# Kernel optimization log

Measured on AMD Instinct MI355X. Metric: run time of the kernel, lower is better.

Reference implementation:

```python
import jax, jax.numpy as jnp
import numpy as np

B, I, H = 65536, 128, 256


def setup_inputs() -> dict:
    key = jax.random.key(0)
    ks = jax.random.split(key, 8)
    return {
        "x_t": jax.random.normal(ks[0], (B, I), dtype=jnp.float32),
        "delta_t": jax.random.uniform(ks[1], (B, 1), dtype=jnp.float32),
        "h_prev": jax.random.normal(ks[2], (B, H), dtype=jnp.float32),
        "c_prev": jax.random.normal(ks[3], (B, H), dtype=jnp.float32),
        # stacked gate weights, order: s, f, i, T, u, o
        "Wh": jax.random.normal(ks[4], (6, H, H), dtype=jnp.float32) * 0.05,
        "Wx": jax.random.normal(ks[5], (6, H, I), dtype=jnp.float32) * 0.05,
        # s_t-input weights, order: f, i, T, u, o
        "Ws": jax.random.normal(ks[6], (5, H, H), dtype=jnp.float32) * 0.05,
        "Wst": jax.random.normal(ks[7], (H, 1), dtype=jnp.float32) * 0.05,
        "b": jnp.zeros((6, H), dtype=jnp.float32),
    }


def reference(x_t, delta_t, h_prev, c_prev, Wh, Wx, Ws, Wst, b):
    # Batched GEMMs over the 6 gates (nn.Linear: y = x @ W.T)
    pre_h = jnp.einsum('bi,goi->gbo', h_prev, Wh)      # [6,B,H]
    pre_x = jnp.einsum('bi,goi->gbo', x_t, Wx)         # [6,B,H]
    s_t = jnp.tanh(pre_h[0] + pre_x[0] + delta_t @ Wst.T + b[0])
    pre_s = jnp.einsum('bi,goi->gbo', s_t, Ws)         # [5,B,H]
    g = pre_h[1:] + pre_x[1:] + pre_s + b[1:, None, :]  # [5,B,H] f,i,T,u,o
    f_t = jax.nn.sigmoid(g[0])
    i_t = jax.nn.sigmoid(g[1])
    T_t = jax.nn.sigmoid(g[2])
    zeta = jnp.tanh(g[3])
    o_t = jax.nn.sigmoid(g[4])
    c_t = f_t * c_prev + i_t * zeta + T_t * s_t
    h_tilde = o_t * jnp.tanh(c_t)
    return (h_tilde, c_t)
```

## Files before the change

### kernel.cpp

```cpp
#include <hip/hip_runtime.h>
#include <hip/hip_bf16.h>


constexpr int Btot = 65536;
constexpr int H    = 256;
constexpr int I    = 128;
constexpr int K1   = 384;
constexpr int BT   = 32;
constexpr int NTHR = 512;
constexpr int SOFF = 24576;

typedef __bf16 bf16x8  __attribute__((ext_vector_type(8)));
typedef float  f32x16  __attribute__((ext_vector_type(16)));
typedef float  f32x4v  __attribute__((ext_vector_type(4)));
typedef unsigned short ushort8 __attribute__((ext_vector_type(8)));

__device__ __forceinline__ unsigned short f2bf(float f) {
    unsigned u = __builtin_bit_cast(unsigned, f);
    u += 0x7fffu + ((u >> 16) & 1u);
    return (unsigned short)(u >> 16);
}
__device__ __forceinline__ float bf2f(unsigned short s) {
    return __builtin_bit_cast(float, ((unsigned)s) << 16);
}
__device__ __forceinline__ float sigm(float x) {
    return __builtin_amdgcn_rcpf(1.0f + exp2f(-1.4426950408889634f * x));
}
__device__ __forceinline__ float tanh_f(float x) {
    return 1.0f - 2.0f * __builtin_amdgcn_rcpf(1.0f + exp2f(2.8853900817779268f * x));
}

__global__ void convert_w(const float* __restrict__ Wh, const float* __restrict__ Wx,
                          const float* __restrict__ Ws, unsigned short* __restrict__ w0,
                          unsigned short* __restrict__ wg) {
    const int t  = blockIdx.x * blockDim.x + threadIdx.x;
    const int N0 = 48 * 2048;
    const int N1 = 5 * 80 * 2048;
    if (t < N0) {
        const int k8 = t >> 11, rem = t & 2047;
        const int col = rem >> 3, e = rem & 7;
        const int k = k8 * 8 + e;
        const float v = (k < H) ? Wh[col * H + k] : Wx[col * I + (k - H)];
        w0[t] = f2bf(v);
    } else if (t < N0 + N1) {
        const int u   = t - N0;
        const int g1  = u / 163840;
        const int rem = u - g1 * 163840;
        const int k8  = rem >> 11;
        const int r2  = rem & 2047;
        const int col = r2 >> 3, e = r2 & 7;
        const int k   = k8 * 8 + e;
        const int g   = g1 + 1;
        float v;
        if (k < H)        v = Wh[g * H * H + col * H + k];
        else if (k < K1)  v = Wx[g * H * I + col * I + (k - H)];
        else              v = Ws[g1 * H * H + col * H + (k - K1)];
        wg[u] = f2bf(v);
    }
}

template<int NIT>
__device__ __forceinline__ void gemm1(const unsigned char* Ab, int abase,
        const unsigned short* __restrict__ Wp, f32x16& acc) {
    bf16x8 b[2], a[2];
    #pragma unroll
    for (int i = 0; i < 2; ++i) {
        b[i] = *(const bf16x8*)(Wp + i * 4096);
        a[i] = *(const bf16x8*)(Ab + abase + i * 1024);
    }
    #pragma unroll
    for (int i = 0; i < NIT; ++i) {
        const bf16x8 av = a[i & 1], bv = b[i & 1];
        if (i + 2 < NIT) {
            a[i & 1] = *(const bf16x8*)(Ab + abase + (i + 2) * 1024);
            b[i & 1] = *(const bf16x8*)(Wp + (i + 2) * 4096);
        }
        acc = __builtin_amdgcn_mfma_f32_32x32x16_bf16(av, bv, acc, 0, 0, 0);
    }
}

__global__ __launch_bounds__(NTHR, 4) void thlstm_fused(
        const float* __restrict__ x_t, const float* __restrict__ delta_t,
        const float* __restrict__ h_prev, const float* __restrict__ c_prev,
        const float* __restrict__ Wst, const float* __restrict__ bias,
        const unsigned short* __restrict__ w0, const unsigned short* __restrict__ wg,
        float* __restrict__ out) {
    __shared__ __align__(16) unsigned char Abuf[40960];
    const int tid = threadIdx.x;
    const int b0  = blockIdx.x * BT;

    #pragma unroll
    for (int it = 0; it < 3; ++it) {
        const int c   = it * NTHR + tid;
        const int k8  = c >> 5, row = c & 31;
        const float* src = (k8 < 32) ? (h_prev + (size_t)(b0 + row) * H + k8 * 8)
                                     : (x_t    + (size_t)(b0 + row) * I + (k8 - 32) * 8);
        const f32x4v v0 = __builtin_nontemporal_load((const f32x4v*)src);
        const f32x4v v1 = __builtin_nontemporal_load(((const f32x4v*)src) + 1);
        ushort8 p;
        p[0] = f2bf(v0[0]); p[1] = f2bf(v0[1]); p[2] = f2bf(v0[2]); p[3] = f2bf(v0[3]);
        p[4] = f2bf(v1[0]); p[5] = f2bf(v1[1]); p[6] = f2bf(v1[2]); p[7] = f2bf(v1[3]);
        *(ushort8*)(Abuf + (k8 * 32 + row) * 16) = p;
    }
    __syncthreads();

    const int lane  = tid & 63;
    const int wv    = tid >> 6;
    const int half  = lane >> 5;
    const int l31   = lane & 31;
    const int ocol  = wv * 32 + l31;
    const int rbase = 4 * half;
    const int abase = half * 512 + l31 * 16;
    const int wlo   = half * 2048 + ocol * 8;
    const int sbase = SOFF + ((ocol >> 3) * 32) * 16 + (ocol & 7) * 2;

    {
        f32x16 acc;
        #pragma unroll
        for (int r = 0; r < 16; ++r) acc[r] = 0.f;
        gemm1<24>(Abuf, abase, w0 + wlo, acc);
        const float wst = Wst[ocol];
        const float bs  = bias[ocol];
        #pragma unroll
        for (int r = 0; r < 16; ++r) {
            const int mrow = (r & 3) + 8 * (r >> 2) + rbase;
            const float sv = tanh_f(acc[r] + delta_t[b0 + mrow] * wst + bs);
            *(unsigned short*)(Abuf + sbase + mrow * 16) = f2bf(sv);
        }
    }
    __syncthreads();

    float    cacc[16];
    unsigned ipk[8];

    {
        f32x16 ac;
        #pragma unroll
        for (int r = 0; r < 16; ++r) ac[r] = 0.f;
        gemm1<40>(Abuf, abase, wg + 0 * 163840 + wlo, ac);
        const float bg = bias[1 * H + ocol];
        #pragma unroll
        for (int r = 0; r < 16; ++r) {
            const int mrow = (r & 3) + 8 * (r >> 2) + rbase;
            const size_t idx = (size_t)(b0 + mrow) * H + ocol;
            cacc[r] = sigm(ac[r] + bg) * __builtin_nontemporal_load(&c_prev[idx]);
        }
    }
    {
        f32x16 ac;
        #pragma unroll
        for (int r = 0; r < 16; ++r) ac[r] = 0.f;
        gemm1<40>(Abuf, abase, wg + 2 * 163840 + wlo, ac);
        const float bg = bias[3 * H + ocol];
        #pragma unroll
        for (int r = 0; r < 16; ++r) {
            const int mrow = (r & 3) + 8 * (r >> 2) + rbase;
            const float sv = bf2f(*(const unsigned short*)(Abuf + sbase + mrow * 16));
            cacc[r] += sigm(ac[r] + bg) * sv;
        }
    }
    {
        f32x16 ac;
        #pragma unroll
        for (int r = 0; r < 16; ++r) ac[r] = 0.f;
        gemm1<40>(Abuf, abase, wg + 1 * 163840 + wlo, ac);
        const float bg = bias[2 * H + ocol];
        float tmpf = 0.f;
        #pragma unroll
        for (int r = 0; r < 16; ++r) {
            const float sg = sigm(ac[r] + bg);
            if ((r & 1) == 0) tmpf = sg;
            else ipk[r >> 1] = (unsigned)f2bf(tmpf) | ((unsigned)f2bf(sg) << 16);
        }
    }
    {
        f32x16 ac;
        #pragma unroll
        for (int r = 0; r < 16; ++r) ac[r] = 0.f;
        gemm1<40>(Abuf, abase, wg + 3 * 163840 + wlo, ac);
        const float bg = bias[4 * H + ocol];
        #pragma unroll
        for (int r = 0; r < 16; ++r) {
            const float iv = bf2f((unsigned short)((ipk[r >> 1] >> ((r & 1) * 16)) & 0xffffu));
            cacc[r] += iv * tanh_f(ac[r] + bg);
        }
    }
    {
        f32x16 ac;
        #pragma unroll
        for (int r = 0; r < 16; ++r) ac[r] = 0.f;
        gemm1<40>(Abuf, abase, wg + 4 * 163840 + wlo, ac);
        const float bg = bias[5 * H + ocol];
        #pragma unroll
        for (int r = 0; r < 16; ++r) {
            const int mrow = (r & 3) + 8 * (r >> 2) + rbase;
            const size_t idx = (size_t)(b0 + mrow) * H + ocol;
            const float c = cacc[r];
            __builtin_nontemporal_store(sigm(ac[r] + bg) * tanh_f(c), &out[idx]);
            __builtin_nontemporal_store(c, &out[(size_t)Btot * H + idx]);
        }
    }
}

extern "C" void kernel_launch(void* const* d_in, const int* in_sizes, int n_in,
                              void* d_out, int out_size, void* d_ws, size_t ws_size,
                              hipStream_t stream) {
    (void)in_sizes; (void)n_in; (void)out_size; (void)ws_size;
    const float* x_t    = (const float*)d_in[0];
    const float* delta  = (const float*)d_in[1];
    const float* h_prev = (const float*)d_in[2];
    const float* c_prev = (const float*)d_in[3];
    const float* Wh     = (const float*)d_in[4];
    const float* Wx     = (const float*)d_in[5];
    const float* Ws     = (const float*)d_in[6];
    const float* Wst    = (const float*)d_in[7];
    const float* bias   = (const float*)d_in[8];
    float* out = (float*)d_out;

    unsigned short* w0 = (unsigned short*)d_ws;
    unsigned short* wg = w0 + 48 * 2048;

    const int total = 48 * 2048 + 5 * 80 * 2048;
    convert_w<<<(total + 255) / 256, 256, 0, stream>>>(Wh, Wx, Ws, w0, wg);
    thlstm_fused<<<Btot / BT, NTHR, 0, stream>>>(x_t, delta, h_prev, c_prev,
                                                 Wst, bias, w0, wg, out);
}
```

Before: 211.3 us.

## Split GEMM K dimension across wave pairs with LDS partial-sum exchange

Doubles the block to 1024 threads and splits each gate GEMM's K dimension between two waves that share the same output columns. Partial accumulators are written to LDS as bf16, exchanged after a barrier, and each wave finishes half the rows of the epilogue. The aim is shorter per-wave MFMA chains and more waves to hide latency. In exchange it adds a barrier per gate, LDS traffic, bf16 rounding of the partial sums, and raises LDS use to about 104KB, which limits occupancy to one block per CU.

New measurement: 353.9 us. 1.67x slower.

```diff
diff --git a/kernel.cpp b/kernel.cpp
--- a/kernel.cpp
+++ b/kernel.cpp
@@ -7,8 +7,9 @@
 constexpr int I    = 128;
 constexpr int K1   = 384;
 constexpr int BT   = 32;
-constexpr int NTHR = 512;
+constexpr int NTHR = 1024;
 constexpr int SOFF = 24576;
+constexpr int POFF = 40960;
 
 typedef __bf16 bf16x8  __attribute__((ext_vector_type(8)));
 typedef float  f32x16  __attribute__((ext_vector_type(16)));
@@ -79,124 +80,160 @@
     }
 }
 
+__device__ __forceinline__ void combine(unsigned char* Ab, const f32x16& acc,
+        int pw0, int pw1, int prd, int ks, int pp, float full[8]) {
+    ushort8 p0, p1;
+    #pragma unroll
+    for (int j = 0; j < 8; ++j) { p0[j] = f2bf(acc[j]); p1[j] = f2bf(acc[8 + j]); }
+    *(ushort8*)(Ab + pp * 32768 + pw0) = p0;
+    *(ushort8*)(Ab + pp * 32768 + pw1) = p1;
+    __syncthreads();
+    const ushort8 q = *(const ushort8*)(Ab + pp * 32768 + prd);
+    #pragma unroll
+    for (int j = 0; j < 8; ++j) full[j] = acc[ks * 8 + j] + bf2f(q[j]);
+}
+
 __global__ __launch_bounds__(NTHR, 4) void thlstm_fused(
         const float* __restrict__ x_t, const float* __restrict__ delta_t,
         const float* __restrict__ h_prev, const float* __restrict__ c_prev,
         const float* __restrict__ Wst, const float* __restrict__ bias,
         const unsigned short* __restrict__ w0, const unsigned short* __restrict__ wg,
         float* __restrict__ out) {
-    __shared__ __align__(16) unsigned char Abuf[40960];
+    __shared__ __align__(16) unsigned char Abuf[106496];
     const int tid = threadIdx.x;
     const int b0  = blockIdx.x * BT;
 
     #pragma unroll
-    for (int it = 0; it < 3; ++it) {
-        const int c   = it * NTHR + tid;
-        const int k8  = c >> 5, row = c & 31;
-        const float* src = (k8 < 32) ? (h_prev + (size_t)(b0 + row) * H + k8 * 8)
-                                     : (x_t    + (size_t)(b0 + row) * I + (k8 - 32) * 8);
-        const f32x4v v0 = __builtin_nontemporal_load((const f32x4v*)src);
-        const f32x4v v1 = __builtin_nontemporal_load(((const f32x4v*)src) + 1);
-        ushort8 p;
-        p[0] = f2bf(v0[0]); p[1] = f2bf(v0[1]); p[2] = f2bf(v0[2]); p[3] = f2bf(v0[3]);
-        p[4] = f2bf(v1[0]); p[5] = f2bf(v1[1]); p[6] = f2bf(v1[2]); p[7] = f2bf(v1[3]);
-        *(ushort8*)(Abuf + (k8 * 32 + row) * 16) = p;
+    for (int it = 0; it < 2; ++it) {
+        const int c = it * NTHR + tid;
+        if (c < BT * 48) {
+            const int k8 = c >> 5, row = c & 31;
+            const float* src = (k8 < 32) ? (h_prev + (size_t)(b0 + row) * H + k8 * 8)
+                                         : (x_t    + (size_t)(b0 + row) * I + (k8 - 32) * 8);
+            const f32x4v v0 = __builtin_nontemporal_load((const f32x4v*)src);
+            const f32x4v v1 = __builtin_nontemporal_load(((const f32x4v*)src) + 1);
+            ushort8 p;
+            p[0] = f2bf(v0[0]); p[1] = f2bf(v0[1]); p[2] = f2bf(v0[2]); p[3] = f2bf(v0[3]);
+            p[4] = f2bf(v1[0]); p[5] = f2bf(v1[1]); p[6] = f2bf(v1[2]); p[7] = f2bf(v1[3]);
+            *(ushort8*)(Abuf + (k8 * 32 + row) * 16) = p;
+        }
     }
     __syncthreads();
 
     const int lane  = tid & 63;
     const int wv    = tid >> 6;
+    const int cs    = wv >> 1;
+    const int ks    = wv & 1;
     const int half  = lane >> 5;
     const int l31   = lane & 31;
-    const int ocol  = wv * 32 + l31;
+    const int ocol  = cs * 32 + l31;
     const int rbase = 4 * half;
     const int abase = half * 512 + l31 * 16;
     const int wlo   = half * 2048 + ocol * 8;
-    const int sbase = SOFF + ((ocol >> 3) * 32) * 16 + (ocol & 7) * 2;
-
-    {
-        f32x16 acc;
-        #pragma unroll
-        for (int r = 0; r < 16; ++r) acc[r] = 0.f;
-        gemm1<24>(Abuf, abase, w0 + wlo, acc);
+    const int sbase = SOFF + (ocol >> 3) * 512 + (ocol & 7) * 2;
+    const int pw0 = POFF + wv * 1024 + lane * 16;
+    const int pw1 = POFF + 16384 + wv * 1024 + lane * 16;
+    const int prd = POFF + ks * 16384 + (wv ^ 1) * 1024 + lane * 16;
+
+    {
+        f32x16 acc;
+        #pragma unroll
+        for (int r = 0; r < 16; ++r) acc[r] = 0.f;
+        gemm1<12>(Abuf, abase + ks * 12 * 1024, w0 + wlo + ks * 12 * 4096, acc);
+        float full[8];
+        combine(Abuf, acc, pw0, pw1, prd, ks, 0, full);
         const float wst = Wst[ocol];
         const float bs  = bias[ocol];
         #pragma unroll
-        for (int r = 0; r < 16; ++r) {
-            const int mrow = (r & 3) + 8 * (r >> 2) + rbase;
-            const float sv = tanh_f(acc[r] + delta_t[b0 + mrow] * wst + bs);
+        for (int j = 0; j < 8; ++j) {
+            const int r = ks * 8 + j;
+            const int mrow = (r & 3) + 8 * (r >> 2) + rbase;
+            const float sv = tanh_f(full[j] + delta_t[b0 + mrow] * wst + bs);
             *(unsigned short*)(Abuf + sbase + mrow * 16) = f2bf(sv);
         }
     }
     __syncthreads();
 
-    float    cacc[16];
-    unsigned ipk[8];
-
-    {
-        f32x16 ac;
-        #pragma unroll
-        for (int r = 0; r < 16; ++r) ac[r] = 0.f;
-        gemm1<40>(Abuf, abase, wg + 0 * 163840 + wlo, ac);
+    float    cacc[8];
+    unsigned ipk[4];
+
+    {
+        f32x16 acc;
+        #pragma unroll
+        for (int r = 0; r < 16; ++r) acc[r] = 0.f;
+        gemm1<20>(Abuf, abase + ks * 20 * 1024, wg + 0 * 163840 + wlo + ks * 20 * 4096, acc);
+        float full[8];
+        combine(Abuf, acc, pw0, pw1, prd, ks, 1, full);
         const float bg = bias[1 * H + ocol];
         #pragma unroll
-        for (int r = 0; r < 16; ++r) {
+        for (int j = 0; j < 8; ++j) {
+            const int r = ks * 8 + j;
             const int mrow = (r & 3) + 8 * (r >> 2) + rbase;
             const size_t idx = (size_t)(b0 + mrow) * H + ocol;
-            cacc[r] = sigm(ac[r] + bg) * __builtin_nontemporal_load(&c_prev[idx]);
-        }
-    }
-    {
-        f32x16 ac;
-        #pragma unroll
-        for (int r = 0; r < 16; ++r) ac[r] = 0.f;
-        gemm1<40>(Abuf, abase, wg + 2 * 163840 + wlo, ac);
+            cacc[j] = sigm(full[j] + bg) * __builtin_nontemporal_load(&c_prev[idx]);
+        }
+    }
+    {
+        f32x16 acc;
+        #pragma unroll
+        for (int r = 0; r < 16; ++r) acc[r] = 0.f;
+        gemm1<20>(Abuf, abase + ks * 20 * 1024, wg + 2 * 163840 + wlo + ks * 20 * 4096, acc);
+        float full[8];
+        combine(Abuf, acc, pw0, pw1, prd, ks, 0, full);
         const float bg = bias[3 * H + ocol];
         #pragma unroll
-        for (int r = 0; r < 16; ++r) {
+        for (int j = 0; j < 8; ++j) {
+            const int r = ks * 8 + j;
             const int mrow = (r & 3) + 8 * (r >> 2) + rbase;
             const float sv = bf2f(*(const unsigned short*)(Abuf + sbase + mrow * 16));
-            cacc[r] += sigm(ac[r] + bg) * sv;
-        }
-    }
-    {
-        f32x16 ac;
-        #pragma unroll
-        for (int r = 0; r < 16; ++r) ac[r] = 0.f;
-        gemm1<40>(Abuf, abase, wg + 1 * 163840 + wlo, ac);
+            cacc[j] += sigm(full[j] + bg) * sv;
+        }
+    }
+    {
+        f32x16 acc;
+        #pragma unroll
+        for (int r = 0; r < 16; ++r) acc[r] = 0.f;
+        gemm1<20>(Abuf, abase + ks * 20 * 1024, wg + 1 * 163840 + wlo + ks * 20 * 4096, acc);
+        float full[8];
+        combine(Abuf, acc, pw0, pw1, prd, ks, 1, full);
         const float bg = bias[2 * H + ocol];
         float tmpf = 0.f;
         #pragma unroll
-        for (int r = 0; r < 16; ++r) {
-            const float sg = sigm(ac[r] + bg);
-            if ((r & 1) == 0) tmpf = sg;
-            else ipk[r >> 1] = (unsigned)f2bf(tmpf) | ((unsigned)f2bf(sg) << 16);
-        }
-    }
-    {
-        f32x16 ac;
-        #pragma unroll
-        for (int r = 0; r < 16; ++r) ac[r] = 0.f;
-        gemm1<40>(Abuf, abase, wg + 3 * 163840 + wlo, ac);
+        for (int j = 0; j < 8; ++j) {
+            const float sg = sigm(full[j] + bg);
+            if ((j & 1) == 0) tmpf = sg;
+            else ipk[j >> 1] = (unsigned)f2bf(tmpf) | ((unsigned)f2bf(sg) << 16);
+        }
+    }
+    {
+        f32x16 acc;
+        #pragma unroll
+        for (int r = 0; r < 16; ++r) acc[r] = 0.f;
+        gemm1<20>(Abuf, abase + ks * 20 * 1024, wg + 3 * 163840 + wlo + ks * 20 * 4096, acc);
+        float full[8];
+        combine(Abuf, acc, pw0, pw1, prd, ks, 0, full);
         const float bg = bias[4 * H + ocol];
         #pragma unroll
-        for (int r = 0; r < 16; ++r) {
-            const float iv = bf2f((unsigned short)((ipk[r >> 1] >> ((r & 1) * 16)) & 0xffffu));
-            cacc[r] += iv * tanh_f(ac[r] + bg);
-        }
-    }
-    {
-        f32x16 ac;
-        #pragma unroll
-        for (int r = 0; r < 16; ++r) ac[r] = 0.f;
-        gemm1<40>(Abuf, abase, wg + 4 * 163840 + wlo, ac);
+        for (int j = 0; j < 8; ++j) {
+            const float iv = bf2f((unsigned short)((ipk[j >> 1] >> ((j & 1) * 16)) & 0xffffu));
+            cacc[j] += iv * tanh_f(full[j] + bg);
+        }
+    }
+    {
+        f32x16 acc;
+        #pragma unroll
+        for (int r = 0; r < 16; ++r) acc[r] = 0.f;
+        gemm1<20>(Abuf, abase + ks * 20 * 1024, wg + 4 * 163840 + wlo + ks * 20 * 4096, acc);
+        float full[8];
+        combine(Abuf, acc, pw0, pw1, prd, ks, 1, full);
         const float bg = bias[5 * H + ocol];
         #pragma unroll
-        for (int r = 0; r < 16; ++r) {
+        for (int j = 0; j < 8; ++j) {
+            const int r = ks * 8 + j;
             const int mrow = (r & 3) + 8 * (r >> 2) + rbase;
             const size_t idx = (size_t)(b0 + mrow) * H + ocol;
-            const float c = cacc[r];
-            __builtin_nontemporal_store(sigm(ac[r] + bg) * tanh_f(c), &out[idx]);
+            const float c = cacc[j];
+            __builtin_nontemporal_store(sigm(full[j] + bg) * tanh_f(c), &out[idx]);
             __builtin_nontemporal_store(c, &out[(size_t)Btot * H + idx]);
         }
     }
```
